# Kernel optimization log

Measured on AMD Instinct MI355X. Metric: run time of the kernel, lower is better.

Reference implementation:

```python
import jax, jax.numpy as jnp
import numpy as np

ATT = 64   # attention_size (becomes number of split chunks / effective heads)
NH = 16    # num_heads (becomes chunk width / effective head dim)


def setup_inputs() -> dict:
    key = jax.random.key(0)
    ks = jax.random.split(key, 9)
    B, T, E = 4, 1024, 1024
    AH = ATT * NH  # 1024
    s = 0.02
    return {
        "x": jax.random.normal(ks[0], (B, T, E), jnp.float32),
        "Wq": jax.random.normal(ks[1], (E, AH), jnp.float32) * s,
        "bq": jax.random.normal(ks[2], (AH,), jnp.float32) * s,
        "Wk": jax.random.normal(ks[3], (E, AH), jnp.float32) * s,
        "bk": jax.random.normal(ks[4], (AH,), jnp.float32) * s,
        "Wv": jax.random.normal(ks[5], (E, AH), jnp.float32) * s,
        "bv": jax.random.normal(ks[6], (AH,), jnp.float32) * s,
        "Wo": jax.random.normal(ks[7], (AH, E), jnp.float32) * s,
        "bo": jax.random.normal(ks[8], (E,), jnp.float32) * s,
    }


def reference(x, Wq, bq, Wk, bk, Wv, bv, Wo, bo):
    B, T, E = x.shape
    A, H = ATT, NH

    q = x @ Wq + bq  # [B,T,A*H]
    k = x @ Wk + bk
    v = x @ Wv + bv

    # torch.split(m, num_heads, dim=2) -> A chunks of width H; cat along dim 0
    def split_cat(m):
        # [B,T,A,H] -> [A,B,T,H] -> [A*B,T,H]
        return m.reshape(B, T, A, H).transpose(2, 0, 1, 3).reshape(A * B, T, H)

    q = split_cat(q)
    k = split_cat(k)
    v = split_cat(v)

    scores = jnp.einsum('bqh,bkh->bqk', q, k) / (A ** 0.5)  # [A*B,T,T]
    attn = jax.nn.softmax(scores, axis=-1)
    z = jnp.einsum('bqk,bkh->bqh', attn, v)  # [A*B,T,H]

    # faithful to torch: contiguous [A*B,T,H] viewed as [B, T, A*H] (no un-permute)
    z = z.reshape(B, T, A * H)
    return z @ Wo + bo
```

## Files before the change

### kernel.cpp

```cpp
#include <hip/hip_runtime.h>
#include <hip/hip_bf16.h>


typedef __bf16 bf16_t;
typedef bf16_t bf16x8 __attribute__((ext_vector_type(8)));
typedef short  s16x4 __attribute__((ext_vector_type(4)));
typedef float  f32x4 __attribute__((ext_vector_type(4)));

#define SCALE_LOG2E 0.18033688011112042f

__device__ __forceinline__ void async16(const bf16_t* g, void* l) {
    __builtin_amdgcn_global_load_lds(
        (const __attribute__((address_space(1))) unsigned int*)g,
        (__attribute__((address_space(3))) unsigned int*)l,
        16, 0, 0);
}

__global__ __launch_bounds__(256) void cast_f32_bf16(
    const float* __restrict__ in, bf16_t* __restrict__ out, int n8)
{
    int i = blockIdx.x * 256 + threadIdx.x;
    if (i >= n8) return;
    const float4* p = (const float4*)in + (size_t)i * 2;
    float4 a = p[0], b = p[1];
    bf16x8 o;
    o[0] = (bf16_t)a.x; o[1] = (bf16_t)a.y; o[2] = (bf16_t)a.z; o[3] = (bf16_t)a.w;
    o[4] = (bf16_t)b.x; o[5] = (bf16_t)b.y; o[6] = (bf16_t)b.z; o[7] = (bf16_t)b.w;
    *((bf16x8*)out + i) = o;
}

__global__ __launch_bounds__(256) void transpose_cast(
    const float* __restrict__ W0, const float* __restrict__ W1,
    const float* __restrict__ W2, const float* __restrict__ W3,
    bf16_t* __restrict__ out)
{
    __shared__ float st[32][33];
    const float* W = (blockIdx.z == 0) ? W0 : (blockIdx.z == 1) ? W1
                   : (blockIdx.z == 2) ? W2 : W3;
    bf16_t* o = out + (size_t)blockIdx.z * 1024 * 1024;
    const int n0 = blockIdx.x * 32, k0 = blockIdx.y * 32;
    const int t = threadIdx.x;
    const int r = t >> 3, c4 = (t & 7) * 4;
    float4 v = *(const float4*)(W + (size_t)(k0 + r) * 1024 + n0 + c4);
    st[r][c4 + 0] = v.x; st[r][c4 + 1] = v.y; st[r][c4 + 2] = v.z; st[r][c4 + 3] = v.w;
    __syncthreads();
    bf16_t tmp[4] __attribute__((aligned(8)));
    #pragma unroll
    for (int i = 0; i < 4; ++i) tmp[i] = (bf16_t)st[c4 + i][r];
    *(uint2*)(o + (size_t)(n0 + r) * 1024 + k0 + c4) = *(const uint2*)tmp;
}

template<bool FUSED, int MT>
__global__ __launch_bounds__(256, 3) void gemm_glds(
    const bf16_t* __restrict__ A, const bf16_t* __restrict__ Bt,
    const float* __restrict__ b0, const float* __restrict__ b1,
    const float* __restrict__ b2,
    bf16_t* __restrict__ Qo, bf16_t* __restrict__ Ko, bf16_t* __restrict__ Vo,
    float* __restrict__ Fo)
{
    const int K = 1024;
    __shared__ __align__(16) bf16_t As[MT * 32];
    __shared__ __align__(16) bf16_t Bs[128 * 32];

    constexpr int NTPW = (MT == 128) ? 4 : 2;
    constexpr int JA   = MT / 64;

    const int tid  = threadIdx.x;
    const int wave = tid >> 6;
    const int lane = tid & 63;
    const int quad = lane >> 4;
    const int l16  = lane & 15;
    const int m0 = blockIdx.y * MT;
    const int n0 = blockIdx.x * 128;
    const int wm = (MT == 128) ? (wave >> 1) * 64 : 0;
    const int wn = (MT == 128) ? (wave & 1) * 64 : wave * 32;

    int goffA[JA], goffB[2];
    #pragma unroll
    for (int j = 0; j < JA; ++j) {
        const int row = j * 64 + (tid >> 2);
        const int cl  = (tid & 3) ^ ((row >> 1) & 3);
        goffA[j] = (m0 + row) * K + cl * 8;
    }
    #pragma unroll
    for (int j = 0; j < 2; ++j) {
        const int row = j * 64 + (tid >> 2);
        const int cl  = (tid & 3) ^ ((row >> 1) & 3);
        goffB[j] = (n0 + row) * K + cl * 8;
    }
    const int ldsoff = wave * 1024;

    f32x4 acc[4][NTPW] = {};
    const int sw = (l16 >> 1) & 3;

    for (int k0 = 0; k0 < K; k0 += 32) {
        #pragma unroll
        for (int j = 0; j < JA; ++j)
            async16(A + goffA[j] + k0, (char*)As + j * 4096 + ldsoff);
        #pragma unroll
        for (int j = 0; j < 2; ++j)
            async16(Bt + goffB[j] + k0, (char*)Bs + j * 4096 + ldsoff);
        __syncthreads();

        bf16x8 af[4], bfr[NTPW];
        #pragma unroll
        for (int mt = 0; mt < 4; ++mt)
            af[mt] = *(const bf16x8*)(&As[(wm + mt * 16 + l16) * 32 + (quad ^ sw) * 8]);
        #pragma unroll
        for (int nt = 0; nt < NTPW; ++nt)
            bfr[nt] = *(const bf16x8*)(&Bs[(wn + nt * 16 + l16) * 32 + (quad ^ sw) * 8]);
        #pragma unroll
        for (int mt = 0; mt < 4; ++mt)
            #pragma unroll
            for (int nt = 0; nt < NTPW; ++nt)
                acc[mt][nt] = __builtin_amdgcn_mfma_f32_16x16x32_bf16(
                    af[mt], bfr[nt], acc[mt][nt], 0, 0, 0);
        __syncthreads();
    }

    if (FUSED) {
        const int sel = n0 >> 10;
        const float* bias = (sel == 0) ? b0 : (sel == 1) ? b1 : b2;
        bf16_t* Cout      = (sel == 0) ? Qo : (sel == 1) ? Ko : Vo;
        const float scl   = (sel == 1) ? SCALE_LOG2E : 1.0f;
        const int nb = n0 & 1023;
        #pragma unroll
        for (int nt = 0; nt < NTPW; ++nt) {
            const int n = nb + wn + nt * 16 + l16;
            const float bb = bias[n];
            #pragma unroll
            for (int mt = 0; mt < 4; ++mt)
                #pragma unroll
                for (int i = 0; i < 4; ++i) {
                    const int m = m0 + wm + mt * 16 + quad * 4 + i;
                    Cout[(size_t)m * 1024 + n] = (bf16_t)((acc[mt][nt][i] + bb) * scl);
                }
        }
    } else {
        #pragma unroll
        for (int nt = 0; nt < NTPW; ++nt) {
            const int n = n0 + wn + nt * 16 + l16;
            const float bb = b0[n];
            #pragma unroll
            for (int mt = 0; mt < 4; ++mt)
                #pragma unroll
                for (int i = 0; i < 4; ++i) {
                    const int m = m0 + wm + mt * 16 + quad * 4 + i;
                    Fo[(size_t)m * 1024 + n] = acc[mt][nt][i] + bb;
                }
        }
    }
}

__global__ __launch_bounds__(256, 4) void attn_kernel(
    const bf16_t* __restrict__ Q, const bf16_t* __restrict__ K,
    const bf16_t* __restrict__ V, bf16_t* __restrict__ Z)
{
    __shared__ __align__(16) bf16_t Vt[2][16 * 72];

    const int tid  = threadIdx.x;
    const int wave = tid >> 6;
    const int lane = tid & 63;
    const int quad = lane >> 4;
    const int l16  = lane & 15;
    const int hd = blockIdx.x >> 2;
    const int qc = blockIdx.x & 3;
    const int a = hd >> 2, b = hd & 3;
    const int col0 = a * 16;
    const int qbase = qc * 256 + wave * 64;

    bf16x8 qf[4] = {};
    if (quad < 2) {
        #pragma unroll
        for (int qs = 0; qs < 4; ++qs)
            qf[qs] = *(const bf16x8*)(Q +
                (size_t)(b * 1024 + qbase + qs * 16 + l16) * 1024 + col0 + quad * 8);
    }

    const bf16_t* Kp = K + (size_t)(b * 1024 + l16) * 1024 + col0 + quad * 8;
    bf16x8 kf[2][4] = {};
    if (quad < 2) {
        #pragma unroll
        for (int kt = 0; kt < 4; ++kt)
            kf[0][kt] = *(const bf16x8*)(Kp + (size_t)(kt * 16) * 1024);
    }

    const int r  = tid >> 2;
    const int dq = (tid & 3) * 4;
    const bf16_t* Vp = V + (size_t)(b * 1024 + r) * 1024 + col0 + dq;

    uint2 vv = *(const uint2*)Vp;
    {
        bf16_t t4[4] __attribute__((aligned(8)));
        *(uint2*)t4 = vv;
        #pragma unroll
        for (int ii = 0; ii < 4; ++ii)
            Vt[0][(dq + ii) * 72 + r] = t4[ii];
    }
    vv = *(const uint2*)(Vp + (size_t)64 * 1024);
    __syncthreads();

    const s16x4 ones = { 0x3F80, 0x3F80, 0x3F80, 0x3F80 };

    f32x4 zacc[4] = {};
    f32x4 lacc[4] = {};

    #pragma unroll
    for (int j = 0; j < 16; ++j) {
        const int cur = j & 1, nxt = cur ^ 1;

        if (j < 15 && quad < 2) {
            #pragma unroll
            for (int kt = 0; kt < 4; ++kt)
                kf[nxt][kt] = *(const bf16x8*)(Kp + (size_t)((j + 1) * 64 + kt * 16) * 1024);
        }
        if (j < 15) {
            bf16_t t4[4] __attribute__((aligned(8)));
            *(uint2*)t4 = vv;
            #pragma unroll
            for (int ii = 0; ii < 4; ++ii)
                Vt[nxt][(dq + ii) * 72 + r] = t4[ii];
            if (j < 14)
                vv = *(const uint2*)(Vp + (size_t)((j + 2) * 64) * 1024);
        }

        #pragma unroll
        for (int kt = 0; kt < 4; ++kt) {
            const s16x4 vfrag = __builtin_bit_cast(s16x4,
                *(const uint2*)(&Vt[cur][l16 * 72 + kt * 16 + quad * 4]));
            #pragma unroll
            for (int qs = 0; qs < 4; ++qs) {
                f32x4 zc = {0.f, 0.f, 0.f, 0.f};
                f32x4 s = __builtin_amdgcn_mfma_f32_16x16x32_bf16(
                    kf[cur][kt], qf[qs], zc, 0, 0, 0);
                unsigned int u0 = __builtin_bit_cast(unsigned int,
                    __builtin_amdgcn_exp2f(s[0])) + 0x8000u;
                unsigned int u1 = __builtin_bit_cast(unsigned int,
                    __builtin_amdgcn_exp2f(s[1])) + 0x8000u;
                unsigned int u2 = __builtin_bit_cast(unsigned int,
                    __builtin_amdgcn_exp2f(s[2])) + 0x8000u;
                unsigned int u3 = __builtin_bit_cast(unsigned int,
                    __builtin_amdgcn_exp2f(s[3])) + 0x8000u;
                uint2 w;
                w.x = __builtin_amdgcn_perm(u1, u0, 0x07060302u);
                w.y = __builtin_amdgcn_perm(u3, u2, 0x07060302u);
                const s16x4 pfrag = __builtin_bit_cast(s16x4, w);
                zacc[qs] = __builtin_amdgcn_mfma_f32_16x16x16bf16_1k(
                    vfrag, pfrag, zacc[qs], 0, 0, 0);
                lacc[qs] = __builtin_amdgcn_mfma_f32_16x16x16bf16_1k(
                    ones, pfrag, lacc[qs], 0, 0, 0);
            }
        }
        __syncthreads();
    }

    #pragma unroll
    for (int qs = 0; qs < 4; ++qs) {
        const float inv = 1.0f / lacc[qs][0];
        const int q = qbase + qs * 16 + l16;
        bf16_t o4[4] __attribute__((aligned(8)));
        #pragma unroll
        for (int i = 0; i < 4; ++i) o4[i] = (bf16_t)(zacc[qs][i] * inv);
        *(uint2*)(Z + ((size_t)hd * 1024 + q) * 16 + quad * 4) = *(const uint2*)o4;
    }
}

extern "C" void kernel_launch(void* const* d_in, const int* in_sizes, int n_in,
                              void* d_out, int out_size, void* d_ws, size_t ws_size,
                              hipStream_t stream) {
    const float* x  = (const float*)d_in[0];
    const float* Wq = (const float*)d_in[1];
    const float* bq = (const float*)d_in[2];
    const float* Wk = (const float*)d_in[3];
    const float* bk = (const float*)d_in[4];
    const float* Wv = (const float*)d_in[5];
    const float* bv = (const float*)d_in[6];
    const float* Wo = (const float*)d_in[7];
    const float* bo = (const float*)d_in[8];
    float* out = (float*)d_out;

    char* ws = (char*)d_ws;
    bf16_t* x_bf = (bf16_t*)(ws);
    bf16_t* Wt   = (bf16_t*)(ws + (8u << 20));
    bf16_t* Qb   = (bf16_t*)(ws + (16u << 20));
    bf16_t* Kb   = (bf16_t*)(ws + (24u << 20));
    bf16_t* Vb   = (bf16_t*)(ws + (32u << 20));
    bf16_t* Zb   = (bf16_t*)(ws + (40u << 20));
    bf16_t* WtO  = Wt + (size_t)3 * 1024 * 1024;

    cast_f32_bf16<<<dim3(2048), dim3(256), 0, stream>>>(x, x_bf, 524288);
    transpose_cast<<<dim3(32, 32, 4), dim3(256), 0, stream>>>(Wq, Wk, Wv, Wo, Wt);

    gemm_glds<true, 128><<<dim3(24, 32), dim3(256), 0, stream>>>(
        x_bf, Wt, bq, bk, bv, Qb, Kb, Vb, nullptr);

    attn_kernel<<<dim3(1024), dim3(256), 0, stream>>>(Qb, Kb, Vb, Zb);

    gemm_glds<false, 64><<<dim3(8, 64), dim3(256), 0, stream>>>(
        Zb, WtO, bo, nullptr, nullptr, nullptr, nullptr, nullptr, out);
}
```

Measured before the change: 191.2 us.

## Use per-wave V tiles to drop block barriers; use K16 MFMA for scores

Each wave now loads and transposes its own copy of the V tile into a private LDS slice, so the per-iteration __syncthreads is removed. The QK^T product switches from the 16x16x32 MFMA, which was half zero-padded, to the 16x16x16 variant with 4-element Q/K fragments. V fragments are read from LDS before the next tile is written. This trades four times the V global traffic and LDS footprint for no block-wide synchronisation and less MFMA padding waste.

```diff
diff --git a/kernel.cpp b/kernel.cpp
--- a/kernel.cpp
+++ b/kernel.cpp
@@ -156,7 +156,7 @@
     const bf16_t* __restrict__ Q, const bf16_t* __restrict__ K,
     const bf16_t* __restrict__ V, bf16_t* __restrict__ Z)
 {
-    __shared__ __align__(16) bf16_t Vt[2][16 * 72];
+    __shared__ __align__(16) bf16_t Vt[4][2][16 * 72];
 
     const int tid  = threadIdx.x;
     const int wave = tid >> 6;
@@ -169,36 +169,32 @@
     const int col0 = a * 16;
     const int qbase = qc * 256 + wave * 64;
 
-    bf16x8 qf[4] = {};
-    if (quad < 2) {
-        #pragma unroll
-        for (int qs = 0; qs < 4; ++qs)
-            qf[qs] = *(const bf16x8*)(Q +
-                (size_t)(b * 1024 + qbase + qs * 16 + l16) * 1024 + col0 + quad * 8);
-    }
-
-    const bf16_t* Kp = K + (size_t)(b * 1024 + l16) * 1024 + col0 + quad * 8;
-    bf16x8 kf[2][4] = {};
-    if (quad < 2) {
-        #pragma unroll
-        for (int kt = 0; kt < 4; ++kt)
-            kf[0][kt] = *(const bf16x8*)(Kp + (size_t)(kt * 16) * 1024);
-    }
-
-    const int r  = tid >> 2;
-    const int dq = (tid & 3) * 4;
-    const bf16_t* Vp = V + (size_t)(b * 1024 + r) * 1024 + col0 + dq;
-
-    uint2 vv = *(const uint2*)Vp;
+    s16x4 qf[4];
+    #pragma unroll
+    for (int qs = 0; qs < 4; ++qs)
+        qf[qs] = __builtin_bit_cast(s16x4, *(const uint2*)(Q +
+            (size_t)(b * 1024 + qbase + qs * 16 + l16) * 1024 + col0 + quad * 4));
+
+    const bf16_t* Kp = K + (size_t)(b * 1024 + l16) * 1024 + col0 + quad * 4;
+    s16x4 kf[2][4];
+    #pragma unroll
+    for (int kt = 0; kt < 4; ++kt)
+        kf[0][kt] = __builtin_bit_cast(s16x4,
+            *(const uint2*)(Kp + (size_t)(kt * 16) * 1024));
+
+    const bf16_t* Vp = V + (size_t)(b * 1024 + lane) * 1024 + col0;
+    bf16x8 vlo = *(const bf16x8*)(Vp);
+    bf16x8 vhi = *(const bf16x8*)(Vp + 8);
     {
-        bf16_t t4[4] __attribute__((aligned(8)));
-        *(uint2*)t4 = vv;
-        #pragma unroll
-        for (int ii = 0; ii < 4; ++ii)
-            Vt[0][(dq + ii) * 72 + r] = t4[ii];
-    }
-    vv = *(const uint2*)(Vp + (size_t)64 * 1024);
-    __syncthreads();
+        bf16_t* vt0 = &Vt[wave][0][0];
+        #pragma unroll
+        for (int d = 0; d < 8; ++d) {
+            vt0[d * 72 + lane]       = vlo[d];
+            vt0[(d + 8) * 72 + lane] = vhi[d];
+        }
+    }
+    vlo = *(const bf16x8*)(Vp + (size_t)64 * 1024);
+    vhi = *(const bf16x8*)(Vp + (size_t)64 * 1024 + 8);
 
     const s16x4 ones = { 0x3F80, 0x3F80, 0x3F80, 0x3F80 };
 
@@ -209,29 +205,35 @@
     for (int j = 0; j < 16; ++j) {
         const int cur = j & 1, nxt = cur ^ 1;
 
-        if (j < 15 && quad < 2) {
+        s16x4 vfrag[4];
+        #pragma unroll
+        for (int kt = 0; kt < 4; ++kt)
+            vfrag[kt] = __builtin_bit_cast(s16x4, *(const uint2*)(
+                &Vt[wave][cur][l16 * 72 + kt * 16 + quad * 4]));
+
+        if (j < 15) {
+            bf16_t* vtn = &Vt[wave][nxt][0];
+            #pragma unroll
+            for (int d = 0; d < 8; ++d) {
+                vtn[d * 72 + lane]       = vlo[d];
+                vtn[(d + 8) * 72 + lane] = vhi[d];
+            }
+            if (j < 14) {
+                vlo = *(const bf16x8*)(Vp + (size_t)((j + 2) * 64) * 1024);
+                vhi = *(const bf16x8*)(Vp + (size_t)((j + 2) * 64) * 1024 + 8);
+            }
             #pragma unroll
             for (int kt = 0; kt < 4; ++kt)
-                kf[nxt][kt] = *(const bf16x8*)(Kp + (size_t)((j + 1) * 64 + kt * 16) * 1024);
-        }
-        if (j < 15) {
-            bf16_t t4[4] __attribute__((aligned(8)));
-            *(uint2*)t4 = vv;
-            #pragma unroll
-            for (int ii = 0; ii < 4; ++ii)
-                Vt[nxt][(dq + ii) * 72 + r] = t4[ii];
-            if (j < 14)
-                vv = *(const uint2*)(Vp + (size_t)((j + 2) * 64) * 1024);
+                kf[nxt][kt] = __builtin_bit_cast(s16x4, *(const uint2*)(
+                    Kp + (size_t)((j + 1) * 64 + kt * 16) * 1024));
         }
 
         #pragma unroll
         for (int kt = 0; kt < 4; ++kt) {
-            const s16x4 vfrag = __builtin_bit_cast(s16x4,
-                *(const uint2*)(&Vt[cur][l16 * 72 + kt * 16 + quad * 4]));
             #pragma unroll
             for (int qs = 0; qs < 4; ++qs) {
                 f32x4 zc = {0.f, 0.f, 0.f, 0.f};
-                f32x4 s = __builtin_amdgcn_mfma_f32_16x16x32_bf16(
+                f32x4 s = __builtin_amdgcn_mfma_f32_16x16x16bf16_1k(
                     kf[cur][kt], qf[qs], zc, 0, 0, 0);
                 unsigned int u0 = __builtin_bit_cast(unsigned int,
                     __builtin_amdgcn_exp2f(s[0])) + 0x8000u;
@@ -246,12 +248,11 @@
                 w.y = __builtin_amdgcn_perm(u3, u2, 0x07060302u);
                 const s16x4 pfrag = __builtin_bit_cast(s16x4, w);
                 zacc[qs] = __builtin_amdgcn_mfma_f32_16x16x16bf16_1k(
-                    vfrag, pfrag, zacc[qs], 0, 0, 0);
+                    vfrag[kt], pfrag, zacc[qs], 0, 0, 0);
                 lacc[qs] = __builtin_amdgcn_mfma_f32_16x16x16bf16_1k(
                     ones, pfrag, lacc[qs], 0, 0, 0);
             }
         }
-        __syncthreads();
     }
 
     #pragma unroll
```

After: 197.9 us. 3.5% more time.
